# Kernel tuning notes

Measured on AMD Instinct MI355X. Metric: run time of the kernel, lower is better.

## Reference

```python
import jax, jax.numpy as jnp
import numpy as np

# J2 (von Mises) plane-strain elastoplasticity with linear isotropic hardening
# (faithful stand-in for pyprnn's J2Material: elastic predictor + radial return,
#  committed history = plastic strain tensor + accumulated plastic strain).
E_MOD = 3130.0   # Young's modulus (epoxy, MPa)
NU = 0.37        # Poisson ratio
SIG_Y = 64.8     # initial yield stress
H_ISO = 300.0    # linear isotropic hardening modulus
MU = E_MOD / (2.0 * (1.0 + NU))
LAM = E_MOD * NU / ((1.0 + NU) * (1.0 - 2.0 * NU))


def j2_update(eps, eps_p, alpha):
    """eps: [P,3] (exx, eyy, gamma_xy engineering); eps_p: [P,4] (xx,yy,zz,xy tensorial);
    alpha: [P] accumulated plastic strain. Returns (stress [P,3], eps_p_new, alpha_new)."""
    ee_xx = eps[:, 0] - eps_p[:, 0]
    ee_yy = eps[:, 1] - eps_p[:, 1]
    ee_zz = -eps_p[:, 2]                      # plane strain: total ezz = 0
    ee_xy = 0.5 * eps[:, 2] - eps_p[:, 3]     # tensorial shear
    tr = ee_xx + ee_yy + ee_zz
    # trial (elastic predictor) stress
    sxx = LAM * tr + 2.0 * MU * ee_xx
    syy = LAM * tr + 2.0 * MU * ee_yy
    szz = LAM * tr + 2.0 * MU * ee_zz
    sxy = 2.0 * MU * ee_xy
    p = (sxx + syy + szz) / 3.0
    dxx, dyy, dzz = sxx - p, syy - p, szz - p
    q = jnp.sqrt(1.5 * (dxx * dxx + dyy * dyy + dzz * dzz + 2.0 * sxy * sxy))
    f = q - (SIG_Y + H_ISO * alpha)
    dgam = jnp.maximum(f, 0.0) / (3.0 * MU + H_ISO)   # radial return, closed form
    qs = jnp.maximum(q, 1e-12)
    nxx, nyy, nzz, nxy = 1.5 * dxx / qs, 1.5 * dyy / qs, 1.5 * dzz / qs, 1.5 * sxy / qs
    two_mu_dg = 2.0 * MU * dgam
    sig = jnp.stack([sxx - two_mu_dg * nxx, syy - two_mu_dg * nyy, sxy - two_mu_dg * nxy], axis=-1)
    eps_p_new = eps_p + dgam[:, None] * jnp.stack([nxx, nyy, nzz, nxy], axis=-1)
    alpha_new = alpha + dgam
    return sig, eps_p_new, alpha_new


def setup_inputs() -> dict:
    key = jax.random.key(0)
    k1, k2, k3 = jax.random.split(key, 3)
    B, T, F = 16384, 128, 3
    MATPTS = 16
    L, O = MATPTS * F, 3
    x = jax.random.normal(k1, (B, T, F), dtype=jnp.float32) * 0.02  # strain paths
    W1 = jax.random.normal(k2, (L, F), dtype=jnp.float32) * (1.0 / np.sqrt(F))
    W2 = jax.random.normal(k3, (O, L), dtype=jnp.float32) * (1.0 / np.sqrt(L))
    return {"x": x, "W1": W1, "W2": W2}


def reference(x, W1, W2):
    B, T, F = x.shape
    L = W1.shape[0]
    P = B * (L // F)                 # total material points = batch * mat_pts
    W2s = jax.nn.softplus(W2)        # SoftLayer: positive weights, no bias
    xt = jnp.swapaxes(x, 0, 1)       # [T, B, F]

    def step(carry, xi):
        eps_p, alpha = carry
        lat = xi @ W1.T                       # fc1 (no bias): [B, L]
        eps = lat.reshape(P, F)               # per-material-point strain
        sig, eps_p, alpha = j2_update(eps, eps_p, alpha)   # update + commit
        out = sig.reshape(B, L) @ W2s.T       # fc2 softplus-weighted linear
        return (eps_p, alpha), out

    carry0 = (jnp.zeros((P, 4), jnp.float32), jnp.zeros((P,), jnp.float32))
    _, ys = jax.lax.scan(step, carry0, xt)    # ys: [T, B, O]
    return jnp.swapaxes(ys, 0, 1)             # [B, T, O]
```

## Files before the change

kernel.cpp:

```cpp
#include <hip/hip_runtime.h>
#include <math.h>


#define BLOCK 256
#define BPB 32
#define TSTEPS 128
#define ROWF (TSTEPS * 3)

typedef float v2 __attribute__((ext_vector_type(2)));

static __device__ __forceinline__ v2 vfma(v2 a, v2 b, v2 c) {
    return __builtin_elementwise_fma(a, b, c);
}
static __device__ __forceinline__ v2 vmax(v2 a, v2 b) {
    return __builtin_elementwise_max(a, b);
}

#define DPP_ADDST(v, ctrl)                                                   \
    v += __int_as_float(__builtin_amdgcn_update_dpp(                         \
        0, __float_as_int(v), (ctrl), 0xf, 0xf, true))
#define RED8(v)                                                              \
    do { DPP_ADDST(v, 0xB1); DPP_ADDST(v, 0x4E); DPP_ADDST(v, 0x141); } while (0)

#define DPP_ST(r, ctrl) "v_add_f32_dpp %" #r ", %" #r ", %" #r " " ctrl \
                        " row_mask:0xf bank_mask:0xf\n\t"
#define DPP_STAGE24(ctrl) \
    DPP_ST(0, ctrl)  DPP_ST(1, ctrl)  DPP_ST(2, ctrl)  DPP_ST(3, ctrl)  \
    DPP_ST(4, ctrl)  DPP_ST(5, ctrl)  DPP_ST(6, ctrl)  DPP_ST(7, ctrl)  \
    DPP_ST(8, ctrl)  DPP_ST(9, ctrl)  DPP_ST(10, ctrl) DPP_ST(11, ctrl) \
    DPP_ST(12, ctrl) DPP_ST(13, ctrl) DPP_ST(14, ctrl) DPP_ST(15, ctrl) \
    DPP_ST(16, ctrl) DPP_ST(17, ctrl) DPP_ST(18, ctrl) DPP_ST(19, ctrl) \
    DPP_ST(20, ctrl) DPP_ST(21, ctrl) DPP_ST(22, ctrl) DPP_ST(23, ctrl)
#define DPP_BFLY24(a0,a1,a2,a3,a4,a5,a6,a7,a8,a9,a10,a11,                    \
                   a12,a13,a14,a15,a16,a17,a18,a19,a20,a21,a22,a23)          \
  asm volatile(                                                              \
    "s_nop 1\n\t"                                                            \
    DPP_STAGE24("quad_perm:[1,0,3,2]")                                       \
    DPP_STAGE24("quad_perm:[2,3,0,1]")                                       \
    DPP_STAGE24("row_half_mirror")                                           \
    : "+v"(a0), "+v"(a1), "+v"(a2), "+v"(a3), "+v"(a4), "+v"(a5),            \
      "+v"(a6), "+v"(a7), "+v"(a8), "+v"(a9), "+v"(a10), "+v"(a11),          \
      "+v"(a12), "+v"(a13), "+v"(a14), "+v"(a15), "+v"(a16), "+v"(a17),      \
      "+v"(a18), "+v"(a19), "+v"(a20), "+v"(a21), "+v"(a22), "+v"(a23))

__global__ __launch_bounds__(BLOCK, 2)
void prnn_j2_kernel(const float* __restrict__ x,
                    const float* __restrict__ W1,
                    const float* __restrict__ W2,
                    float* __restrict__ out)
{
    constexpr float MU    = (float)(3130.0 / (2.0 * (1.0 + 0.37)));
    constexpr float LAM   = (float)(3130.0 * 0.37 / ((1.0 + 0.37) * (1.0 - 2.0 * 0.37)));
    constexpr float SIG_Y = 64.8f;
    constexpr float H_ISO = 300.0f;
    const float TWO_MU  = 2.0f * MU;
    const float INV_DEN = 1.0f / (3.0f * MU + H_ISO);
    const float K3P     = (3.0f * MU) * INV_DEN;
    const float HP      = H_ISO * INV_DEN;
    const float CSC     = 1.0f / (MU * 2.4494897427831781f);
    const float Y0      = SIG_Y * CSC;
    const float SQRT2   = 1.41421356237309515f;
    const float RSQRT2  = 0.70710678118654752f;

    const int tid = threadIdx.x;
    const int g   = tid >> 3;
    const int l   = tid & 7;
    const int gb  = blockIdx.x * BPB + g;

    const float* xb = x + gb * ROWF;
    float* ob = out + gb * ROWF;

    const int pa = l, pb = l + 8;
    v2 w1r0[3], w1r1[3], w1h2[3];
    #pragma unroll
    for (int f = 0; f < 3; ++f) {
        w1r0[f].x = W1[(3 * pa + 0) * 3 + f];
        w1r0[f].y = W1[(3 * pb + 0) * 3 + f];
        w1r1[f].x = W1[(3 * pa + 1) * 3 + f];
        w1r1[f].y = W1[(3 * pb + 1) * 3 + f];
        w1h2[f].x = 0.5f * W1[(3 * pa + 2) * 3 + f];
        w1h2[f].y = 0.5f * W1[(3 * pb + 2) * 3 + f];
    }
    v2 w2p[3][3];
    #pragma unroll
    for (int o = 0; o < 3; ++o)
        #pragma unroll
        for (int c = 0; c < 3; ++c) {
            float wa = W2[o * 48 + 3 * pa + c];
            float wb = W2[o * 48 + 3 * pb + c];
            w2p[o][c].x = fmaxf(wa, 0.0f) + log1pf(expf(-fabsf(wa)));
            w2p[o][c].y = fmaxf(wb, 0.0f) + log1pf(expf(-fabsf(wb)));
        }

    float Mrow[3];
    {
        float Ms[3][3];
        #pragma unroll
        for (int f = 0; f < 3; ++f) {
            v2 ax = (LAM + TWO_MU) * w1r0[f] + LAM * w1r1[f];
            v2 ay = LAM * w1r0[f] + (LAM + TWO_MU) * w1r1[f];
            v2 as = TWO_MU * w1h2[f];
            #pragma unroll
            for (int o = 0; o < 3; ++o) {
                v2 mp = vfma(w2p[o][0], ax, vfma(w2p[o][1], ay, w2p[o][2] * as));
                float ms = mp.x + mp.y;
                RED8(ms);
                Ms[o][f] = ms;
            }
        }
        #pragma unroll
        for (int f = 0; f < 3; ++f) {
            float v = (l == 0) ? Ms[0][f] : ((l == 1) ? Ms[1][f] : Ms[2][f]);
            Mrow[f] = v;
        }
    }

    v2 wdx[3], wdy[3], wsh[3];
    #pragma unroll
    for (int f = 0; f < 3; ++f) {
        wdx[f] = (2.0f * w1r0[f] - w1r1[f]) * (1.0f / 3.0f);
        wdy[f] = (2.0f * w1r1[f] - w1r0[f]) * (1.0f / 3.0f);
        wsh[f] = SQRT2 * w1h2[f];
    }
    #pragma unroll
    for (int o = 0; o < 3; ++o) w2p[o][2] *= RSQRT2;

    v2 p0 = {0.f,0.f}, p1 = {0.f,0.f}, ps = {0.f,0.f};
    v2 Y  = {Y0, Y0};
    v2 z0 = {0.f,0.f}, z1 = {0.f,0.f}, z2 = {0.f,0.f};

    const float4* xv = (const float4*)xb;
    const bool wact = (l < 3);
    float* obl = ob + l;

#define J2_PHYS(x0_, x1_, x2_, rr, mxv)                                      \
  {                                                                          \
    const float x0s = (x0_), x1s = (x1_), x2s = (x2_);                       \
    const v2 x0 = {x0s, x0s}, x1 = {x1s, x1s}, x2 = {x2s, x2s};              \
    const v2 ex0 = vfma(wdx[0], x0, vfma(wdx[1], x1, wdx[2] * x2));          \
    const v2 ey0 = vfma(wdy[0], x0, vfma(wdy[1], x1, wdy[2] * x2));          \
    const v2 wsy = vfma(wsh[0], x0, vfma(wsh[1], x1, wsh[2] * x2));          \
    const v2 exd = ex0 - p0;                                                 \
    const v2 eyd = ey0 - p1;                                                 \
    const v2 exy = wsy - ps;                                                 \
    const v2 szd = exd + eyd;                             \
    const v2 ua = vfma(eyd, eyd, exd * exd);                                 \
    const v2 ub = vfma(exy, exy, szd * szd);                                 \
    v2 u = ua + ub;                                                          \
    u = vmax(u, (v2){1e-30f, 1e-30f});                                       \
    v2 rq;                                                                   \
    rq.x = __builtin_amdgcn_rsqf(u.x);                                       \
    rq.y = __builtin_amdgcn_rsqf(u.y);                                       \
    const v2 gm = vmax(vfma(-Y, rq, (v2){1.0f, 1.0f}), (v2){0.0f, 0.0f});    \
    const v2 su = u * rq;                    \
    const v2 k  = K3P * gm;                                                  \
    Y = vfma((v2){HP, HP}, gm * su, Y);        \
    const v2 kdx = k * exd;                                                  \
    const v2 kdy = k * eyd;                                                  \
    const v2 kdp = k * exy;                                                  \
    p0 += kdx;                                                               \
    p1 += kdy;                                                               \
    ps += kdp;                                                               \
    z0 = vfma(w2p[0][0], kdx, vfma(w2p[0][1], kdy, vfma(w2p[0][2], kdp, z0)));\
    z1 = vfma(w2p[1][0], kdx, vfma(w2p[1][1], kdy, vfma(w2p[1][2], kdp, z1)));\
    z2 = vfma(w2p[2][0], kdx, vfma(w2p[2][1], kdy, vfma(w2p[2][2], kdp, z2)));\
    (rr)[0] = z0.x + z0.y;                                                   \
    (rr)[1] = z1.x + z1.y;                                                   \
    (rr)[2] = z2.x + z2.y;                                                   \
    (mxv) = fmaf(Mrow[0], x0s, fmaf(Mrow[1], x1s, Mrow[2] * x2s));           \
  }

    float4 A0 = xv[0], A1 = xv[1], A2 = xv[2];
    float4 A3 = xv[3], A4 = xv[4], A5 = xv[5];

    for (int tb = 0; tb < TSTEPS / 8; ++tb) {
        const int nb = (tb < TSTEPS / 8 - 1) ? (6 * tb + 6) : (6 * tb);
        float4 An0 = xv[nb + 0];
        float4 An1 = xv[nb + 1];
        float4 An2 = xv[nb + 2];
        float4 An3 = xv[nb + 3];
        float4 An4 = xv[nb + 4];
        float4 An5 = xv[nb + 5];

        float r[24], mx[8];
        J2_PHYS(A0.x, A0.y, A0.z, r + 0,  mx[0]);
        J2_PHYS(A0.w, A1.x, A1.y, r + 3,  mx[1]);
        J2_PHYS(A1.z, A1.w, A2.x, r + 6,  mx[2]);
        J2_PHYS(A2.y, A2.z, A2.w, r + 9,  mx[3]);
        J2_PHYS(A3.x, A3.y, A3.z, r + 12, mx[4]);
        J2_PHYS(A3.w, A4.x, A4.y, r + 15, mx[5]);
        J2_PHYS(A4.z, A4.w, A5.x, r + 18, mx[6]);
        J2_PHYS(A5.y, A5.z, A5.w, r + 21, mx[7]);

        DPP_BFLY24(r[0],  r[1],  r[2],  r[3],  r[4],  r[5],
                   r[6],  r[7],  r[8],  r[9],  r[10], r[11],
                   r[12], r[13], r[14], r[15], r[16], r[17],
                   r[18], r[19], r[20], r[21], r[22], r[23]);

        if (wact) {
            #pragma unroll
            for (int s = 0; s < 8; ++s) {
                float zz = (l == 0) ? r[3*s] : ((l == 1) ? r[3*s+1] : r[3*s+2]);
                obl[24 * tb + 3 * s] = fmaf(-TWO_MU, zz, mx[s]);
            }
        }

        A0 = An0; A1 = An1; A2 = An2;
        A3 = An3; A4 = An4; A5 = An5;
    }
#undef J2_PHYS
}

extern "C" void kernel_launch(void* const* d_in, const int* in_sizes, int n_in,
                              void* d_out, int out_size, void* d_ws, size_t ws_size,
                              hipStream_t stream) {
    const float* x  = (const float*)d_in[0];
    const float* W1 = (const float*)d_in[1];
    const float* W2 = (const float*)d_in[2];
    float* out = (float*)d_out;

    const int B = 16384;
    dim3 grid(B / BPB);
    dim3 block(BLOCK);
    prnn_j2_kernel<<<grid, block, 0, stream>>>(x, W1, W2, out);
}
```

Measured before the change: 116.5 us.

## Process two batch rows per thread group to interleave independent recurrences

Each 8-lane group now handles two batch samples (A and B) at once, interleaving their serial per-timestep J2 updates so the two independent dependency chains can hide each other's latency. Block count halves (64 batches per block) and launch bounds drop to one block per SIMD slot, which allows more registers per thread. The cost is roughly doubled register pressure and fewer resident waves, so occupancy-based latency hiding is traded for instruction-level parallelism.

```diff
diff --git a/kernel.cpp b/kernel.cpp
--- a/kernel.cpp
+++ b/kernel.cpp
@@ -3,7 +3,7 @@
 
 
 #define BLOCK 256
-#define BPB 32
+#define BPB 64
 #define TSTEPS 128
 #define ROWF (TSTEPS * 3)
 
@@ -43,7 +43,7 @@
       "+v"(a12), "+v"(a13), "+v"(a14), "+v"(a15), "+v"(a16), "+v"(a17),      \
       "+v"(a18), "+v"(a19), "+v"(a20), "+v"(a21), "+v"(a22), "+v"(a23))
 
-__global__ __launch_bounds__(BLOCK, 2)
+__global__ __launch_bounds__(BLOCK, 1)
 void prnn_j2_kernel(const float* __restrict__ x,
                     const float* __restrict__ W1,
                     const float* __restrict__ W2,
@@ -65,10 +65,13 @@
     const int tid = threadIdx.x;
     const int g   = tid >> 3;
     const int l   = tid & 7;
-    const int gb  = blockIdx.x * BPB + g;
-
-    const float* xb = x + gb * ROWF;
-    float* ob = out + gb * ROWF;
+    const int gbA = blockIdx.x * BPB + g;
+    const int gbB = gbA + 32;
+
+    const float* xbA = x + gbA * ROWF;
+    const float* xbB = x + gbB * ROWF;
+    float* obA = out + gbA * ROWF;
+    float* obB = out + gbB * ROWF;
 
     const int pa = l, pb = l + 8;
     v2 w1r0[3], w1r1[3], w1h2[3];
@@ -125,24 +128,29 @@
     #pragma unroll
     for (int o = 0; o < 3; ++o) w2p[o][2] *= RSQRT2;
 
-    v2 p0 = {0.f,0.f}, p1 = {0.f,0.f}, ps = {0.f,0.f};
-    v2 Y  = {Y0, Y0};
-    v2 z0 = {0.f,0.f}, z1 = {0.f,0.f}, z2 = {0.f,0.f};
-
-    const float4* xv = (const float4*)xb;
+    v2 pA0 = {0.f,0.f}, pA1 = {0.f,0.f}, pAs = {0.f,0.f};
+    v2 YA  = {Y0, Y0};
+    v2 zA0 = {0.f,0.f}, zA1 = {0.f,0.f}, zA2 = {0.f,0.f};
+    v2 pB0 = {0.f,0.f}, pB1 = {0.f,0.f}, pBs = {0.f,0.f};
+    v2 YB  = {Y0, Y0};
+    v2 zB0 = {0.f,0.f}, zB1 = {0.f,0.f}, zB2 = {0.f,0.f};
+
+    const float4* xvA = (const float4*)xbA;
+    const float4* xvB = (const float4*)xbB;
     const bool wact = (l < 3);
-    float* obl = ob + l;
-
-#define J2_PHYS(x0_, x1_, x2_, rr, mxv)                                      \
+    float* oblA = obA + l;
+    float* oblB = obB + l;
+
+#define J2_PHYS(P0, P1, PS, YY, Z0, Z1, Z2, x0_, x1_, x2_, rr, mxv)          \
   {                                                                          \
     const float x0s = (x0_), x1s = (x1_), x2s = (x2_);                       \
     const v2 x0 = {x0s, x0s}, x1 = {x1s, x1s}, x2 = {x2s, x2s};              \
     const v2 ex0 = vfma(wdx[0], x0, vfma(wdx[1], x1, wdx[2] * x2));          \
     const v2 ey0 = vfma(wdy[0], x0, vfma(wdy[1], x1, wdy[2] * x2));          \
     const v2 wsy = vfma(wsh[0], x0, vfma(wsh[1], x1, wsh[2] * x2));          \
-    const v2 exd = ex0 - p0;                                                 \
-    const v2 eyd = ey0 - p1;                                                 \
-    const v2 exy = wsy - ps;                                                 \
+    const v2 exd = ex0 - P0;                                                 \
+    const v2 eyd = ey0 - P1;                                                 \
+    const v2 exy = wsy - PS;                                                 \
     const v2 szd = exd + eyd;                             \
     const v2 ua = vfma(eyd, eyd, exd * exd);                                 \
     const v2 ub = vfma(exy, exy, szd * szd);                                 \
@@ -151,63 +159,76 @@
     v2 rq;                                                                   \
     rq.x = __builtin_amdgcn_rsqf(u.x);                                       \
     rq.y = __builtin_amdgcn_rsqf(u.y);                                       \
-    const v2 gm = vmax(vfma(-Y, rq, (v2){1.0f, 1.0f}), (v2){0.0f, 0.0f});    \
+    const v2 gm = vmax(vfma(-YY, rq, (v2){1.0f, 1.0f}), (v2){0.0f, 0.0f});   \
     const v2 su = u * rq;                    \
     const v2 k  = K3P * gm;                                                  \
-    Y = vfma((v2){HP, HP}, gm * su, Y);        \
+    YY = vfma((v2){HP, HP}, gm * su, YY);      \
     const v2 kdx = k * exd;                                                  \
     const v2 kdy = k * eyd;                                                  \
     const v2 kdp = k * exy;                                                  \
-    p0 += kdx;                                                               \
-    p1 += kdy;                                                               \
-    ps += kdp;                                                               \
-    z0 = vfma(w2p[0][0], kdx, vfma(w2p[0][1], kdy, vfma(w2p[0][2], kdp, z0)));\
-    z1 = vfma(w2p[1][0], kdx, vfma(w2p[1][1], kdy, vfma(w2p[1][2], kdp, z1)));\
-    z2 = vfma(w2p[2][0], kdx, vfma(w2p[2][1], kdy, vfma(w2p[2][2], kdp, z2)));\
-    (rr)[0] = z0.x + z0.y;                                                   \
-    (rr)[1] = z1.x + z1.y;                                                   \
-    (rr)[2] = z2.x + z2.y;                                                   \
+    P0 += kdx;                                                               \
+    P1 += kdy;                                                               \
+    PS += kdp;                                                               \
+    Z0 = vfma(w2p[0][0], kdx, vfma(w2p[0][1], kdy, vfma(w2p[0][2], kdp, Z0)));\
+    Z1 = vfma(w2p[1][0], kdx, vfma(w2p[1][1], kdy, vfma(w2p[1][2], kdp, Z1)));\
+    Z2 = vfma(w2p[2][0], kdx, vfma(w2p[2][1], kdy, vfma(w2p[2][2], kdp, Z2)));\
+    (rr)[0] = Z0.x + Z0.y;                                                   \
+    (rr)[1] = Z1.x + Z1.y;                                                   \
+    (rr)[2] = Z2.x + Z2.y;                                                   \
     (mxv) = fmaf(Mrow[0], x0s, fmaf(Mrow[1], x1s, Mrow[2] * x2s));           \
   }
 
-    float4 A0 = xv[0], A1 = xv[1], A2 = xv[2];
-    float4 A3 = xv[3], A4 = xv[4], A5 = xv[5];
+#define STEP_A(X0, X1, X2, s) \
+    J2_PHYS(pA0, pA1, pAs, YA, zA0, zA1, zA2, X0, X1, X2, rA + 3*(s), mxA[s])
+#define STEP_B(X0, X1, X2, s) \
+    J2_PHYS(pB0, pB1, pBs, YB, zB0, zB1, zB2, X0, X1, X2, rB + 3*(s), mxB[s])
+
+    float4 A0 = xvA[0], A1 = xvA[1], A2 = xvA[2];
+    float4 A3 = xvA[3], A4 = xvA[4], A5 = xvA[5];
+    float4 B0 = xvB[0], B1 = xvB[1], B2 = xvB[2];
+    float4 B3 = xvB[3], B4 = xvB[4], B5 = xvB[5];
 
     for (int tb = 0; tb < TSTEPS / 8; ++tb) {
         const int nb = (tb < TSTEPS / 8 - 1) ? (6 * tb + 6) : (6 * tb);
-        float4 An0 = xv[nb + 0];
-        float4 An1 = xv[nb + 1];
-        float4 An2 = xv[nb + 2];
-        float4 An3 = xv[nb + 3];
-        float4 An4 = xv[nb + 4];
-        float4 An5 = xv[nb + 5];
-
-        float r[24], mx[8];
-        J2_PHYS(A0.x, A0.y, A0.z, r + 0,  mx[0]);
-        J2_PHYS(A0.w, A1.x, A1.y, r + 3,  mx[1]);
-        J2_PHYS(A1.z, A1.w, A2.x, r + 6,  mx[2]);
-        J2_PHYS(A2.y, A2.z, A2.w, r + 9,  mx[3]);
-        J2_PHYS(A3.x, A3.y, A3.z, r + 12, mx[4]);
-        J2_PHYS(A3.w, A4.x, A4.y, r + 15, mx[5]);
-        J2_PHYS(A4.z, A4.w, A5.x, r + 18, mx[6]);
-        J2_PHYS(A5.y, A5.z, A5.w, r + 21, mx[7]);
-
-        DPP_BFLY24(r[0],  r[1],  r[2],  r[3],  r[4],  r[5],
-                   r[6],  r[7],  r[8],  r[9],  r[10], r[11],
-                   r[12], r[13], r[14], r[15], r[16], r[17],
-                   r[18], r[19], r[20], r[21], r[22], r[23]);
+        float4 An0 = xvA[nb + 0], An1 = xvA[nb + 1], An2 = xvA[nb + 2];
+        float4 An3 = xvA[nb + 3], An4 = xvA[nb + 4], An5 = xvA[nb + 5];
+        float4 Bn0 = xvB[nb + 0], Bn1 = xvB[nb + 1], Bn2 = xvB[nb + 2];
+        float4 Bn3 = xvB[nb + 3], Bn4 = xvB[nb + 4], Bn5 = xvB[nb + 5];
+
+        float rA[24], mxA[8], rB[24], mxB[8];
+        STEP_A(A0.x, A0.y, A0.z, 0);  STEP_B(B0.x, B0.y, B0.z, 0);
+        STEP_A(A0.w, A1.x, A1.y, 1);  STEP_B(B0.w, B1.x, B1.y, 1);
+        STEP_A(A1.z, A1.w, A2.x, 2);  STEP_B(B1.z, B1.w, B2.x, 2);
+        STEP_A(A2.y, A2.z, A2.w, 3);  STEP_B(B2.y, B2.z, B2.w, 3);
+        STEP_A(A3.x, A3.y, A3.z, 4);  STEP_B(B3.x, B3.y, B3.z, 4);
+        STEP_A(A3.w, A4.x, A4.y, 5);  STEP_B(B3.w, B4.x, B4.y, 5);
+        STEP_A(A4.z, A4.w, A5.x, 6);  STEP_B(B4.z, B4.w, B5.x, 6);
+        STEP_A(A5.y, A5.z, A5.w, 7);  STEP_B(B5.y, B5.z, B5.w, 7);
+
+        DPP_BFLY24(rA[0],  rA[1],  rA[2],  rA[3],  rA[4],  rA[5],
+                   rA[6],  rA[7],  rA[8],  rA[9],  rA[10], rA[11],
+                   rA[12], rA[13], rA[14], rA[15], rA[16], rA[17],
+                   rA[18], rA[19], rA[20], rA[21], rA[22], rA[23]);
+        DPP_BFLY24(rB[0],  rB[1],  rB[2],  rB[3],  rB[4],  rB[5],
+                   rB[6],  rB[7],  rB[8],  rB[9],  rB[10], rB[11],
+                   rB[12], rB[13], rB[14], rB[15], rB[16], rB[17],
+                   rB[18], rB[19], rB[20], rB[21], rB[22], rB[23]);
 
         if (wact) {
             #pragma unroll
             for (int s = 0; s < 8; ++s) {
-                float zz = (l == 0) ? r[3*s] : ((l == 1) ? r[3*s+1] : r[3*s+2]);
-                obl[24 * tb + 3 * s] = fmaf(-TWO_MU, zz, mx[s]);
+                float za = (l == 0) ? rA[3*s] : ((l == 1) ? rA[3*s+1] : rA[3*s+2]);
+                float zb = (l == 0) ? rB[3*s] : ((l == 1) ? rB[3*s+1] : rB[3*s+2]);
+                oblA[24 * tb + 3 * s] = fmaf(-TWO_MU, za, mxA[s]);
+                oblB[24 * tb + 3 * s] = fmaf(-TWO_MU, zb, mxB[s]);
             }
         }
 
-        A0 = An0; A1 = An1; A2 = An2;
-        A3 = An3; A4 = An4; A5 = An5;
-    }
+        A0 = An0; A1 = An1; A2 = An2; A3 = An3; A4 = An4; A5 = An5;
+        B0 = Bn0; B1 = Bn1; B2 = Bn2; B3 = Bn3; B4 = Bn4; B5 = Bn5;
+    }
+#undef STEP_A
+#undef STEP_B
 #undef J2_PHYS
 }
 
```

Result: no change. 115.0 us (-1.2%).
